# Kernel optimization log

Measured on AMD Instinct MI355X. Metric: run time of the kernel, lower is better.

The kernel has to match this reference:

```python
import jax, jax.numpy as jnp
import numpy as np
import math

H, KV, D, HID, WIN = 8, 4, 256, 2048, 1024  # heads, kv heads, head_dim, hidden, sliding window
B, S = 1, 2048

def _rms(x, scale):
    # Gemma3RMSNorm: hardcoded 1e-6 eps, (1+scale) gain
    var = jnp.mean(jnp.square(x), axis=-1, keepdims=True)
    return x * jax.lax.rsqrt(var + 1e-6) * (1.0 + scale)

def _rot_half(x):
    x1, x2 = jnp.split(x, 2, axis=-1)
    return jnp.concatenate((-x2, x1), axis=-1)

def setup_inputs() -> dict:
    key = jax.random.key(0)
    ks = jax.random.split(key, 8)
    x = jax.random.normal(ks[0], (B, S, HID), jnp.float32)
    attn_mask = jnp.ones((B, S), jnp.bool_)
    segment_pos = jnp.broadcast_to(jnp.arange(S, dtype=jnp.int32)[None], (B, S))
    # true RoPE tables, theta=1e6 (Gemma3 global layers)
    inv_freq = 1.0 / (1e6 ** (np.arange(0, D, 2, dtype=np.float32) / D))
    ang = np.arange(S, dtype=np.float32)[:, None] * inv_freq[None, :]  # [S, D/2]
    emb = np.concatenate([ang, ang], axis=-1)                          # [S, D]
    cos = jnp.asarray(np.cos(emb), jnp.float32)[None]                  # [1, S, D]
    sin = jnp.asarray(np.sin(emb), jnp.float32)[None]
    sd = 1.0 / math.sqrt(HID)
    wq = jax.random.normal(ks[1], (HID, H * D), jnp.float32) * sd
    wk = jax.random.normal(ks[2], (HID, KV * D), jnp.float32) * sd
    wv = jax.random.normal(ks[3], (HID, KV * D), jnp.float32) * sd
    wo = jax.random.normal(ks[4], (H * D, HID), jnp.float32) * (1.0 / math.sqrt(H * D))
    q_scale = jnp.zeros((D,), jnp.float32)  # zeros_init as in module
    k_scale = jnp.zeros((D,), jnp.float32)
    return dict(x=x, attn_mask=attn_mask, segment_pos=segment_pos, cos=cos, sin=sin,
                wq=wq, wk=wk, wv=wv, wo=wo, q_scale=q_scale, k_scale=k_scale)

def reference(x, attn_mask, segment_pos, cos, sin, wq, wk, wv, wo, q_scale, k_scale):
    b, s, _ = x.shape
    # projections -> [b, h, s, d]
    q = (x @ wq).reshape(b, s, H, D).transpose(0, 2, 1, 3)
    k = (x @ wk).reshape(b, s, KV, D).transpose(0, 2, 1, 3)
    v = (x @ wv).reshape(b, s, KV, D).transpose(0, 2, 1, 3)
    # per-head QK RMSNorm
    q = _rms(q, q_scale)
    k = _rms(k, k_scale)
    # RoPE (cos/sin broadcast over head axis, unsqueeze_dim=1)
    c, sn = cos[:, None], sin[:, None]
    q = q * c + _rot_half(q) * sn
    k = k * c + _rot_half(k) * sn
    # GQA: repeat-interleave kv heads
    rep = H // KV
    k = jnp.repeat(k, rep, axis=1)
    v = jnp.repeat(v, rep, axis=1)
    scores = jnp.einsum('bhqd,bhkd->bhqk', q, k) / math.sqrt(D)
    # causal + padding mask (q_len > 1 path, no image bidirectional mask)
    causal = jnp.tril(jnp.ones((s, s), jnp.bool_))
    mask = causal[None] & attn_mask[:, None, :]          # [b, q, kv]
    # sliding window mask (prefill: cache positions = arange)
    kvpos = jnp.arange(s)
    pos = segment_pos[:, :, None]
    sliding = (kvpos[None, None] > pos - WIN) & (kvpos[None, None] < pos + WIN)
    full = mask & sliding
    scores = scores + jnp.where(full[:, None], 0.0, -1e37)
    w = jax.nn.softmax(scores.astype(jnp.float32), axis=-1).astype(scores.dtype)
    out = jnp.einsum('bhqk,bhkd->bhqd', w, v)
    out = out.transpose(0, 2, 1, 3).reshape(b, s, H * D)
    return out @ wo
```

## Files before the change

kernel.cpp:

```cpp
#include <hip/hip_runtime.h>
#include <hip/hip_bf16.h>

#define S_LEN 2048
#define HID 2048
#define NH 8
#define NKV 4
#define HD 256
#define WIN 1024

typedef __hip_bfloat16 bf16;
typedef __attribute__((ext_vector_type(8))) short bf16x8;
typedef __attribute__((ext_vector_type(4))) float f32x4;

__device__ __forceinline__ void gld_lds16(void* lds, const void* g) {
    __builtin_amdgcn_global_load_lds(
        (const __attribute__((address_space(1))) unsigned int*)g,
        (__attribute__((address_space(3))) unsigned int*)lds,
        16, 0, 0);
}


__device__ __forceinline__ void transT_body(const float* __restrict__ src, bf16* __restrict__ dst,
                                            int R, int C, int r0, int c0) {
    __shared__ bf16 Ts[64][72];
    const int tid = threadIdx.x;
    {
        const int r = tid >> 2;
        const int cq = (tid & 3) * 16;
#pragma unroll
        for (int j = 0; j < 16; j += 4) {
            float4 v = *(const float4*)&src[(size_t)(r0 + r) * C + c0 + cq + j];
            Ts[cq + j + 0][r] = __float2bfloat16(v.x);
            Ts[cq + j + 1][r] = __float2bfloat16(v.y);
            Ts[cq + j + 2][r] = __float2bfloat16(v.z);
            Ts[cq + j + 3][r] = __float2bfloat16(v.w);
        }
    }
    __syncthreads();
    {
        const int c = tid >> 2;
        const int rq = (tid & 3) * 16;
#pragma unroll
        for (int j = 0; j < 16; j += 8)
            *(uint4*)&dst[(size_t)(c0 + c) * R + r0 + rq + j] = *(const uint4*)&Ts[c][rq + j];
    }
}

__global__ __launch_bounds__(256)
void prep_all(const float* __restrict__ xf, const float* __restrict__ wqf,
              const float* __restrict__ wkf, const float* __restrict__ wvf,
              bf16* __restrict__ xb, bf16* __restrict__ wqkvt) {
    const int bid = blockIdx.x;
    if (bid < 2048) {
        const int i = bid * 256 + threadIdx.x;
        float4 a = ((const float4*)xf)[i * 2];
        float4 b = ((const float4*)xf)[i * 2 + 1];
        union { uint4 v; bf16 h[8]; } u;
        u.h[0] = __float2bfloat16(a.x); u.h[1] = __float2bfloat16(a.y);
        u.h[2] = __float2bfloat16(a.z); u.h[3] = __float2bfloat16(a.w);
        u.h[4] = __float2bfloat16(b.x); u.h[5] = __float2bfloat16(b.y);
        u.h[6] = __float2bfloat16(b.z); u.h[7] = __float2bfloat16(b.w);
        ((uint4*)xb)[i] = u.v;
    } else {
        const int t = bid - 2048;
        const int bx = t & 63, by = t >> 6;
        const float* src; int C, c0, drow0;
        if (bx < 32)      { src = wqf; C = 2048; c0 = bx * 64;        drow0 = bx * 64; }
        else if (bx < 48) { src = wkf; C = 1024; c0 = (bx - 32) * 64; drow0 = 2048 + (bx - 32) * 64; }
        else              { src = wvf; C = 1024; c0 = (bx - 48) * 64; drow0 = 3072 + (bx - 48) * 64; }
        bf16* dshift = wqkvt + ((size_t)drow0 - c0) * HID;
        transT_body(src, dshift, HID, C, by * 64, c0);
    }
}

__global__ __launch_bounds__(256)
void prep_wo(const float* __restrict__ wof, bf16* __restrict__ wot) {
    const int bx = blockIdx.x & 31, by = blockIdx.x >> 5;
    transT_body(wof, wot, NH * HD, HID, by * 64, bx * 64);
}

__global__ __launch_bounds__(512, 2)
void gemm_qkv8(const bf16* __restrict__ A, const bf16* __restrict__ Bt,
               bf16* __restrict__ P) {
    extern __shared__ bf16 smem[];
    const int tid = threadIdx.x;
    const int w = tid >> 6, lane = tid & 63;
    const int lnm = lane & 15, quad = lane >> 4;
    const int wr = w >> 2, wc = w & 3;
    const int K = 2048;
    const int nt = 16;

    const int bid = blockIdx.x;
    const int xcd = bid & 7, idx = bid >> 3;
    const int wg = xcd * 32 + idx;
    const int z = wg >> 7;
    const int rem = wg & 127;
    const int m0 = (rem >> 4) * 256, n0 = (rem & 15) * 256, kbeg = z * 1024;

    const int sr = lane >> 3;
    const int su = (lane & 7) ^ sr;
    const bf16* gA = A  + (size_t)(m0 + w * 8 + sr) * K + kbeg + su * 8;
    const bf16* gB = Bt + (size_t)(n0 + w * 8 + sr) * K + kbeg + su * 8;
    bf16* const lA = smem + w * 8 * 64;
    bf16* const lB = smem + 32768 + w * 8 * 64;

#define SG_A(d, c, t_) gld_lds16(lA + (d) * 16384 + (c) * 64 * 64, \
                                 gA + (size_t)((c) * 64) * K + (t_) * 64)
#define SG_B(d, c, t_) gld_lds16(lB + (d) * 16384 + (c) * 64 * 64, \
                                 gB + (size_t)((c) * 64) * K + (t_) * 64)
#define AFR(d, m, kh) (*(const bf16x8*)(smem + (d) * 16384 + \
        (wr * 128 + (m) * 16 + lnm) * 64 + (((((kh) << 2) | quad) ^ (lnm & 7)) << 3)))
#define BFR(d, n, kh) (*(const bf16x8*)(smem + 32768 + (d) * 16384 + \
        (wc * 64 + (n) * 16 + lnm) * 64 + (((((kh) << 2) | quad) ^ (lnm & 7)) << 3)))

    f32x4 acc[8][4];
#pragma unroll
    for (int i = 0; i < 8; ++i)
#pragma unroll
        for (int j = 0; j < 4; ++j) acc[i][j] = (f32x4){0.f, 0.f, 0.f, 0.f};

    SG_A(0, 0, 0); SG_A(0, 2, 0);
    SG_B(0, 0, 0); SG_B(0, 1, 0); SG_B(0, 2, 0); SG_B(0, 3, 0);
    SG_A(0, 1, 0); SG_A(0, 3, 0);
    asm volatile("s_waitcnt vmcnt(2)" ::: "memory");
    __builtin_amdgcn_sched_barrier(0);
    __builtin_amdgcn_s_barrier();

    bf16x8 a[2][2], b[4][2];
    for (int t = 0; t < nt; ++t) {
        const int cur = t & 1, nxt = cur ^ 1;
        const bool pf = (t + 1 < nt);

#pragma unroll
        for (int n = 0; n < 4; ++n)
#pragma unroll
            for (int kh = 0; kh < 2; ++kh) b[n][kh] = BFR(cur, n, kh);
#pragma unroll
        for (int m = 0; m < 2; ++m)
#pragma unroll
            for (int kh = 0; kh < 2; ++kh) a[m][kh] = AFR(cur, m, kh);
        if (pf) { SG_A(nxt, 0, t + 1); SG_A(nxt, 2, t + 1); }
        __builtin_amdgcn_s_barrier();
        asm volatile("s_waitcnt lgkmcnt(0)" ::: "memory");
        __builtin_amdgcn_sched_barrier(0);
        __builtin_amdgcn_s_setprio(1);
#pragma unroll
        for (int kh = 0; kh < 2; ++kh)
#pragma unroll
            for (int m = 0; m < 2; ++m)
#pragma unroll
                for (int n = 0; n < 4; ++n)
                    acc[m][n] = __builtin_amdgcn_mfma_f32_16x16x32_bf16(
                        a[m][kh], b[n][kh], acc[m][n], 0, 0, 0);
        __builtin_amdgcn_s_setprio(0);
        __builtin_amdgcn_s_barrier();

#pragma unroll
        for (int m = 0; m < 2; ++m)
#pragma unroll
            for (int kh = 0; kh < 2; ++kh) a[m][kh] = AFR(cur, m + 2, kh);
        if (pf) { SG_B(nxt, 0, t + 1); SG_B(nxt, 1, t + 1); }
        __builtin_amdgcn_s_barrier();
        asm volatile("s_waitcnt lgkmcnt(0)" ::: "memory");
        __builtin_amdgcn_sched_barrier(0);
        __builtin_amdgcn_s_setprio(1);
#pragma unroll
        for (int kh = 0; kh < 2; ++kh)
#pragma unroll
            for (int m = 0; m < 2; ++m)
#pragma unroll
                for (int n = 0; n < 4; ++n)
                    acc[m + 2][n] = __builtin_amdgcn_mfma_f32_16x16x32_bf16(
                        a[m][kh], b[n][kh], acc[m + 2][n], 0, 0, 0);
        __builtin_amdgcn_s_setprio(0);
        if (pf) { asm volatile("s_waitcnt vmcnt(4)" ::: "memory"); }
        else    { asm volatile("s_waitcnt vmcnt(0)" ::: "memory"); }
        __builtin_amdgcn_sched_barrier(0);
        __builtin_amdgcn_s_barrier();

#pragma unroll
        for (int m = 0; m < 2; ++m)
#pragma unroll
            for (int kh = 0; kh < 2; ++kh) a[m][kh] = AFR(cur, m + 4, kh);
        if (pf) { SG_B(nxt, 2, t + 1); SG_B(nxt, 3, t + 1); }
        __builtin_amdgcn_s_barrier();
        asm volatile("s_waitcnt lgkmcnt(0)" ::: "memory");
        __builtin_amdgcn_sched_barrier(0);
        __builtin_amdgcn_s_setprio(1);
#pragma unroll
        for (int kh = 0; kh < 2; ++kh)
#pragma unroll
            for (int m = 0; m < 2; ++m)
#pragma unroll
                for (int n = 0; n < 4; ++n)
                    acc[m + 4][n] = __builtin_amdgcn_mfma_f32_16x16x32_bf16(
                        a[m][kh], b[n][kh], acc[m + 4][n], 0, 0, 0);
        __builtin_amdgcn_s_setprio(0);
        __builtin_amdgcn_s_barrier();

#pragma unroll
        for (int m = 0; m < 2; ++m)
#pragma unroll
            for (int kh = 0; kh < 2; ++kh) a[m][kh] = AFR(cur, m + 6, kh);
        if (pf) { SG_A(nxt, 1, t + 1); SG_A(nxt, 3, t + 1); }
        __builtin_amdgcn_s_barrier();
        asm volatile("s_waitcnt lgkmcnt(0)" ::: "memory");
        __builtin_amdgcn_sched_barrier(0);
        __builtin_amdgcn_s_setprio(1);
#pragma unroll
        for (int kh = 0; kh < 2; ++kh)
#pragma unroll
            for (int m = 0; m < 2; ++m)
#pragma unroll
                for (int n = 0; n < 4; ++n)
                    acc[m + 6][n] = __builtin_amdgcn_mfma_f32_16x16x32_bf16(
                        a[m][kh], b[n][kh], acc[m + 6][n], 0, 0, 0);
        __builtin_amdgcn_s_setprio(0);
        if (pf) {
            asm volatile("s_waitcnt vmcnt(2)" ::: "memory");
            __builtin_amdgcn_sched_barrier(0);
        }
        __builtin_amdgcn_s_barrier();
    }
#undef SG_A
#undef SG_B
#undef AFR
#undef BFR

    bf16* pqk = P + (size_t)z * 8388608;
    bf16* pvt = pqk + 6291456;
#pragma unroll
    for (int m = 0; m < 8; ++m)
#pragma unroll
        for (int n = 0; n < 4; ++n)
#pragma unroll
            for (int r = 0; r < 4; ++r) {
                const int row = m0 + wr * 128 + m * 16 + quad * 4 + r;
                const int col = n0 + wc * 64 + n * 16 + lnm;
                const float v = acc[m][n][r];
                if (col < 3072) pqk[(size_t)row * 3072 + col] = __float2bfloat16(v);
                else            pvt[(size_t)(col - 3072) * 2048 + row] = __float2bfloat16(v);
            }
}

__global__ __launch_bounds__(256)
void qkv_combine(const bf16* __restrict__ P, bf16* __restrict__ Qb,
                 bf16* __restrict__ Kb, bf16* __restrict__ Vtb) {
    const int bid = blockIdx.x;
    union { uint4 v; bf16 h[8]; } a, b, o;
    if (bid < 3072) {
        const unsigned i = bid * 256u + threadIdx.x;
        a.v = *(const uint4*)(P + (size_t)i * 8);
        b.v = *(const uint4*)(P + 8388608 + (size_t)i * 8);
        const unsigned off = i * 8u, row = off / 3072u, col = off - row * 3072u;
        bf16* dst = (col < 2048) ? (Qb + (size_t)row * 2048 + col)
                                 : (Kb + (size_t)row * 1024 + (col - 2048));
#pragma unroll
        for (int j = 0; j < 8; ++j) o.h[j] = __float2bfloat16((float)a.h[j] + (float)b.h[j]);
        *(uint4*)dst = o.v;
    } else {
        const unsigned i = (bid - 3072) * 256u + threadIdx.x;
        a.v = *(const uint4*)(P + 6291456 + (size_t)i * 8);
        b.v = *(const uint4*)(P + 8388608 + 6291456 + (size_t)i * 8);
#pragma unroll
        for (int j = 0; j < 8; ++j) o.h[j] = __float2bfloat16((float)a.h[j] + (float)b.h[j]);
        *(uint4*)(Vtb + (size_t)i * 8) = o.v;
    }
}

template<int MODE>
__global__ __launch_bounds__(512, 2)
void gemm8p(const bf16* __restrict__ A, const bf16* __restrict__ Bt,
            bf16* __restrict__ Cb,
            bf16* __restrict__ Qo, bf16* __restrict__ Ko, bf16* __restrict__ Vto) {
    extern __shared__ bf16 smem[];
    bf16* AsP = smem;
    bf16* BsP = smem + 3 * 256 * 64;

    const int tid = threadIdx.x;
    const int w = tid >> 6, lane = tid & 63;
    const int lnm = lane & 15, quad = lane >> 4;
    const int wr = w >> 1, wc = w & 1;
    const int r8 = lane >> 3;
    const int swz = ((lane & 7) ^ r8) * 8;

    const int bid = blockIdx.x;
    const int xcd = bid & 7, idx = bid >> 3;
    int m0, n0, kbeg, nt;
    size_t zoff = 0;
    {
        const int z   = xcd >> 2;
        const int n_t = (xcd & 3) * 4 + (idx & 3);
        const int m_t = idx >> 2;
        m0 = m_t * 256; n0 = n_t * 128; kbeg = z * 1024; nt = 1024 / 64;
        zoff = (size_t)z * 2048 * 2048;
    }
    const int K = 2048;

    const bf16* pA[4];
#pragma unroll
    for (int g = 0; g < 4; ++g)
        pA[g] = A + (size_t)(m0 + w * 32 + g * 8 + r8) * K + kbeg + swz;
    const bf16* pB[2];
#pragma unroll
    for (int g = 0; g < 2; ++g)
        pB[g] = Bt + (size_t)(n0 + w * 16 + g * 8 + r8) * K + kbeg + swz;
    const int dA = w * 32 * 64;
    const int dB = w * 16 * 64;

#define STG_A(slot, g, t) gld_lds16(AsP + (slot) * 16384 + dA + (g) * 512, pA[g] + (t) * 64)
#define STG_B(slot, g, t) gld_lds16(BsP + (slot) * 8192  + dB + (g) * 512, pB[g] + (t) * 64)
#define LDFRAG(base, row, kh) \
    (*(const bf16x8*)((base) + (row) * 64 + (((((kh) << 2) | quad) ^ ((row) & 7)) << 3)))

    f32x4 acc[4][4];
#pragma unroll
    for (int i = 0; i < 4; ++i)
#pragma unroll
        for (int j = 0; j < 4; ++j) acc[i][j] = (f32x4){0.f, 0.f, 0.f, 0.f};

    STG_A(0, 0, 0); STG_A(0, 1, 0); STG_A(0, 2, 0); STG_A(0, 3, 0);
    STG_B(0, 0, 0); STG_B(0, 1, 0);
    STG_A(1, 0, 1); STG_A(1, 1, 1); STG_A(1, 2, 1); STG_A(1, 3, 1);
    STG_B(1, 0, 1); STG_B(1, 1, 1);
    asm volatile("s_waitcnt vmcnt(6)" ::: "memory");
    __builtin_amdgcn_sched_barrier(0);
    __builtin_amdgcn_s_barrier();

    int sc = 0;
    for (int t = 0; t < nt; ++t) {
        const int ss = (sc == 0) ? 2 : sc - 1;
        const bf16* As_ = AsP + sc * 16384;
        const bf16* Bs_ = BsP + sc * 8192;
        const bool pf = (t + 2 < nt);

        bf16x8 a0[2][2], b[4][2];
#pragma unroll
        for (int tm = 0; tm < 2; ++tm)
#pragma unroll
            for (int kh = 0; kh < 2; ++kh)
                a0[tm][kh] = LDFRAG(As_, wr * 64 + tm * 16 + lnm, kh);
#pragma unroll
        for (int tn = 0; tn < 4; ++tn)
#pragma unroll
            for (int kh = 0; kh < 2; ++kh)
                b[tn][kh] = LDFRAG(Bs_, wc * 64 + tn * 16 + lnm, kh);
        if (pf) { STG_A(ss, 0, t + 2); STG_A(ss, 1, t + 2); STG_B(ss, 0, t + 2); }
        __builtin_amdgcn_s_barrier();
        asm volatile("s_waitcnt lgkmcnt(0)" ::: "memory");
        __builtin_amdgcn_sched_barrier(0);
        __builtin_amdgcn_s_setprio(1);
#pragma unroll
        for (int kh = 0; kh < 2; ++kh)
#pragma unroll
            for (int tm = 0; tm < 2; ++tm)
#pragma unroll
                for (int tn = 0; tn < 4; ++tn)
                    acc[tm][tn] = __builtin_amdgcn_mfma_f32_16x16x32_bf16(
                        a0[tm][kh], b[tn][kh], acc[tm][tn], 0, 0, 0);
        __builtin_amdgcn_s_setprio(0);
        __builtin_amdgcn_s_barrier();

        bf16x8 a1[2][2];
#pragma unroll
        for (int tm = 0; tm < 2; ++tm)
#pragma unroll
            for (int kh = 0; kh < 2; ++kh)
                a1[tm][kh] = LDFRAG(As_, wr * 64 + (tm + 2) * 16 + lnm, kh);
        if (pf) { STG_A(ss, 2, t + 2); STG_A(ss, 3, t + 2); STG_B(ss, 1, t + 2); }
        if (pf) { asm volatile("s_waitcnt vmcnt(6)" ::: "memory"); }
        else    { asm volatile("s_waitcnt vmcnt(0)" ::: "memory"); }
        __builtin_amdgcn_sched_barrier(0);
        __builtin_amdgcn_s_barrier();
        asm volatile("s_waitcnt lgkmcnt(0)" ::: "memory");
        __builtin_amdgcn_sched_barrier(0);
        __builtin_amdgcn_s_setprio(1);
#pragma unroll
        for (int kh = 0; kh < 2; ++kh)
#pragma unroll
            for (int tm = 0; tm < 2; ++tm)
#pragma unroll
                for (int tn = 0; tn < 4; ++tn)
                    acc[tm + 2][tn] = __builtin_amdgcn_mfma_f32_16x16x32_bf16(
                        a1[tm][kh], b[tn][kh], acc[tm + 2][tn], 0, 0, 0);
        __builtin_amdgcn_s_setprio(0);
        __builtin_amdgcn_s_barrier();

        sc = (sc == 2) ? 0 : sc + 1;
    }
#undef STG_A
#undef STG_B
#undef LDFRAG

#pragma unroll
    for (int tm = 0; tm < 4; ++tm)
#pragma unroll
        for (int tn = 0; tn < 4; ++tn)
#pragma unroll
            for (int r = 0; r < 4; ++r) {
                const int row = m0 + wr * 64 + tm * 16 + quad * 4 + r;
                const int col = n0 + wc * 64 + tn * 16 + lnm;
                Cb[zoff + (size_t)row * 2048 + col] = __float2bfloat16(acc[tm][tn][r]);
            }
}

__global__ __launch_bounds__(256)
void splitk_add(const bf16* __restrict__ p, float* __restrict__ out) {
    const int i = blockIdx.x * 256 + threadIdx.x;
    union { uint4 v; bf16 h[8]; } a, b;
    a.v = ((const uint4*)p)[i];
    b.v = ((const uint4*)(p + (size_t)2048 * 2048))[i];
    float4 o0, o1;
    o0.x = (float)a.h[0] + (float)b.h[0]; o0.y = (float)a.h[1] + (float)b.h[1];
    o0.z = (float)a.h[2] + (float)b.h[2]; o0.w = (float)a.h[3] + (float)b.h[3];
    o1.x = (float)a.h[4] + (float)b.h[4]; o1.y = (float)a.h[5] + (float)b.h[5];
    o1.z = (float)a.h[6] + (float)b.h[6]; o1.w = (float)a.h[7] + (float)b.h[7];
    ((float4*)out)[i * 2]     = o0;
    ((float4*)out)[i * 2 + 1] = o1;
}

__global__ __launch_bounds__(64)
void rmsrope_kernel(bf16* __restrict__ Q, bf16* __restrict__ Kb,
                    const float* __restrict__ cosb, const float* __restrict__ sinb,
                    const float* __restrict__ qscale, const float* __restrict__ kscale,
                    float qmul) {
    const int p = blockIdx.x;
    const int hg = blockIdx.y;
    const int lane = threadIdx.x;

    bf16* base;
    const float* scale;
    float mul;
    if (hg < NH) { base = Q + (size_t)p * (NH * HD) + hg * HD; scale = qscale; mul = qmul; }
    else         { base = Kb + (size_t)p * (NKV * HD) + (hg - NH) * HD; scale = kscale; mul = 1.f; }

    const int d0 = lane * 2;
    float x0 = (float)base[d0],       x1 = (float)base[d0 + 1];
    float y0 = (float)base[d0 + 128], y1 = (float)base[d0 + 129];

    float ss = x0 * x0 + x1 * x1 + y0 * y0 + y1 * y1;
#pragma unroll
    for (int off = 32; off > 0; off >>= 1) ss += __shfl_xor(ss, off, 64);
    const float r = rsqrtf(ss * (1.0f / (float)HD) + 1e-6f);

    x0 *= r * (1.f + scale[d0]);
    x1 *= r * (1.f + scale[d0 + 1]);
    y0 *= r * (1.f + scale[d0 + 128]);
    y1 *= r * (1.f + scale[d0 + 129]);

    const size_t cb = (size_t)p * HD;
    const float c0 = cosb[cb + d0],       c1 = cosb[cb + d0 + 1];
    const float cA = cosb[cb + d0 + 128], cB = cosb[cb + d0 + 129];
    const float s0 = sinb[cb + d0],       s1 = sinb[cb + d0 + 1];
    const float sA = sinb[cb + d0 + 128], sB = sinb[cb + d0 + 129];

    base[d0]       = __float2bfloat16((x0 * c0 - y0 * s0) * mul);
    base[d0 + 1]   = __float2bfloat16((x1 * c1 - y1 * s1) * mul);
    base[d0 + 128] = __float2bfloat16((y0 * cA + x0 * sA) * mul);
    base[d0 + 129] = __float2bfloat16((y1 * cB + x1 * sB) * mul);
}

#define NCHUNK 4

__device__ __forceinline__ unsigned pkbf(float a, float b) {
    union { bf16 h; unsigned short u; } ca, cb;
    ca.h = __float2bfloat16(a); cb.h = __float2bfloat16(b);
    return (unsigned)ca.u | ((unsigned)cb.u << 16);
}

__global__ __launch_bounds__(256)
void attn_mfma(const bf16* __restrict__ Q, const bf16* __restrict__ K,
               const bf16* __restrict__ Vt, bf16* __restrict__ Op,
               float2* __restrict__ ml) {
    __shared__ bf16 Ks[2][32][256];
    __shared__ bf16 Vs[256][32];
    const int qt = blockIdx.x, h = blockIdx.y, chunk = blockIdx.z, kvh = h >> 1;
    const int tid = threadIdx.x, w = tid >> 6, lane = tid & 63;
    const int lnm = lane & 15, quad = lane >> 4;

    bf16x8 qf[8];
    const int qrow = qt * 64 + w * 16 + lnm;
#pragma unroll
    for (int s = 0; s < 8; ++s)
        qf[s] = *(const bf16x8*)&Q[(size_t)qrow * HID + h * HD + s * 32 + quad * 8];

    f32x4 o[16];
#pragma unroll
    for (int i = 0; i < 16; ++i) o[i] = (f32x4){0.f, 0.f, 0.f, 0.f};
    float M = -3e38f, L = 0.f;

    const int ktlo = (qt >= 16) ? (2 * qt - 32) : 0;
    const int kthi = 2 * qt + 1;
    const int ntile = kthi - ktlo + 1;
    const int c0 = ktlo + (chunk * ntile) / NCHUNK;
    const int c1 = ktlo + ((chunk + 1) * ntile) / NCHUNK - 1;

    const int srow = w * 8 + (lane >> 5);
    const int sunit = lane & 31;
    const bf16* kg = K + (size_t)kvh * HD;
    const int vrow = lane >> 2;
    const int vgu  = (lane & 3) ^ ((lane >> 3) & 3);
    const bf16* vsrc = Vt + ((size_t)(kvh * HD + w * 64 + vrow)) * S_LEN + vgu * 8;

#define STAGE_K(kt_, buf_)                                                        \
    {                                                                             \
        _Pragma("unroll")                                                         \
        for (int cc = 0; cc < 4; ++cc) {                                          \
            const int r_ = srow + cc * 2;                                         \
            const int ug_ = sunit ^ (r_ & 7);                                     \
            gld_lds16(&Ks[buf_][w * 8 + cc * 2][0],                               \
                      kg + (size_t)((kt_) * 32 + r_) * (NKV * HD) + ug_ * 8);     \
        }                                                                         \
    }
#define STAGE_V(kt_)                                                              \
    {                                                                             \
        _Pragma("unroll")                                                         \
        for (int cc = 0; cc < 4; ++cc)                                            \
            gld_lds16(&Vs[w * 64 + cc * 16][0],                                   \
                      vsrc + (size_t)cc * 16 * S_LEN + (kt_) * 32);               \
    }
#define KFRAG(buf_, t_, s_) \
    (*(const bf16x8*)&Ks[buf_][(t_) * 16 + lnm][((((s_) * 4 + quad) ^ (lnm & 7)) * 8)])
#define VFRAG(t2_) \
    (*(const bf16x8*)&Vs[(t2_) * 16 + lnm][(quad ^ ((lnm >> 1) & 3)) * 8])

    if (c0 <= c1) {
        STAGE_K(c0, 0);
        asm volatile("s_waitcnt vmcnt(0)" ::: "memory");
        __builtin_amdgcn_sched_barrier(0);
        __builtin_amdgcn_s_barrier();

        for (int kt = c0; kt <= c1; ++kt) {
            const int buf = (kt - c0) & 1;
            STAGE_V(kt);
            if (kt < c1) STAGE_K(kt + 1, buf ^ 1);

            f32x4 s4[2];
            s4[0] = (f32x4){0.f, 0.f, 0.f, 0.f};
            s4[1] = (f32x4){0.f, 0.f, 0.f, 0.f};
            __builtin_amdgcn_s_setprio(1);
#pragma unroll
            for (int t = 0; t < 2; ++t)
#pragma unroll
                for (int s = 0; s < 8; ++s)
                    s4[t] = __builtin_amdgcn_mfma_f32_16x16x32_bf16(
                        KFRAG(buf, t, s), qf[s], s4[t], 0, 0, 0);
            __builtin_amdgcn_s_setprio(0);

#pragma unroll
            for (int t = 0; t < 2; ++t)
#pragma unroll
                for (int r = 0; r < 4; ++r) {
                    const int n_g = kt * 32 + t * 16 + quad * 4 + r;
                    if (n_g > qrow || n_g + (WIN - 1) < qrow) s4[t][r] = -1e30f;
                }

            float mx = fmaxf(fmaxf(fmaxf(s4[0][0], s4[0][1]), fmaxf(s4[0][2], s4[0][3])),
                             fmaxf(fmaxf(s4[1][0], s4[1][1]), fmaxf(s4[1][2], s4[1][3])));
            mx = fmaxf(mx, __shfl_xor(mx, 16, 64));
            mx = fmaxf(mx, __shfl_xor(mx, 32, 64));

            if (!__all(mx <= M + 8.f)) {
                const float Mn = fmaxf(M, mx);
                const float al = __expf(M - Mn);
                M = Mn;
                L *= al;
                float alr[4];
#pragma unroll
                for (int r = 0; r < 4; ++r) alr[r] = __shfl(al, quad * 4 + r, 64);
#pragma unroll
                for (int t2 = 0; t2 < 16; ++t2)
#pragma unroll
                    for (int r = 0; r < 4; ++r) o[t2][r] *= alr[r];
            }

            float rs = 0.f;
            unsigned u00, u01, u10, u11;
            {
                float p0 = __expf(s4[0][0] - M), p1 = __expf(s4[0][1] - M);
                float p2 = __expf(s4[0][2] - M), p3 = __expf(s4[0][3] - M);
                rs += (p0 + p1) + (p2 + p3);
                u00 = pkbf(p0, p1); u01 = pkbf(p2, p3);
                p0 = __expf(s4[1][0] - M); p1 = __expf(s4[1][1] - M);
                p2 = __expf(s4[1][2] - M); p3 = __expf(s4[1][3] - M);
                rs += (p0 + p1) + (p2 + p3);
                u10 = pkbf(p0, p1); u11 = pkbf(p2, p3);
            }
            rs += __shfl_xor(rs, 16, 64);
            rs += __shfl_xor(rs, 32, 64);
            L += rs;

            const int slo = lnm + 16 * (2 * (quad & 1));
            const int shi = slo + 16;
            const int A0 = __shfl((int)u00, slo, 64), A1 = __shfl((int)u01, slo, 64);
            const int A2 = __shfl((int)u00, shi, 64), A3 = __shfl((int)u01, shi, 64);
            const int B0 = __shfl((int)u10, slo, 64), B1 = __shfl((int)u11, slo, 64);
            const int B2 = __shfl((int)u10, shi, 64), B3 = __shfl((int)u11, shi, 64);
            union { bf16x8 v; int i4[4]; } pa;
            pa.i4[0] = (quad < 2) ? A0 : B0;
            pa.i4[1] = (quad < 2) ? A1 : B1;
            pa.i4[2] = (quad < 2) ? A2 : B2;
            pa.i4[3] = (quad < 2) ? A3 : B3;

            if (kt < c1) { asm volatile("s_waitcnt vmcnt(4)" ::: "memory"); }
            else         { asm volatile("s_waitcnt vmcnt(0)" ::: "memory"); }
            __builtin_amdgcn_sched_barrier(0);
            __builtin_amdgcn_s_barrier();

            __builtin_amdgcn_s_setprio(1);
#pragma unroll
            for (int t2 = 0; t2 < 16; ++t2)
                o[t2] = __builtin_amdgcn_mfma_f32_16x16x32_bf16(pa.v, VFRAG(t2), o[t2], 0, 0, 0);
            __builtin_amdgcn_s_setprio(0);

            if (kt < c1) {
                asm volatile("s_waitcnt vmcnt(0) lgkmcnt(0)" ::: "memory");
                __builtin_amdgcn_sched_barrier(0);
                __builtin_amdgcn_s_barrier();
            }
        }
    }
#undef STAGE_K
#undef STAGE_V
#undef KFRAG
#undef VFRAG

    const float rL = (L > 0.f) ? (1.f / L) : 0.f;
    float rr[4];
#pragma unroll
    for (int r = 0; r < 4; ++r) rr[r] = __shfl(rL, quad * 4 + r, 64);
    bf16* Opc = Op + (size_t)chunk * S_LEN * HID;
#pragma unroll
    for (int t2 = 0; t2 < 16; ++t2)
#pragma unroll
        for (int r = 0; r < 4; ++r)
            Opc[(size_t)(qt * 64 + w * 16 + quad * 4 + r) * HID + h * HD + t2 * 16 + lnm] =
                __float2bfloat16(o[t2][r] * rr[r]);
    if (quad == 0)
        ml[((size_t)chunk * S_LEN + qt * 64 + w * 16 + lnm) * NH + h] = make_float2(M, L);
}

__global__ __launch_bounds__(256)
void attn_combine(const bf16* __restrict__ Op, const float2* __restrict__ ml,
                  bf16* __restrict__ O) {
    const int row = blockIdx.x, h = blockIdx.y, d = threadIdx.x;
    float2 c[NCHUNK];
    float Mx = -3e38f;
#pragma unroll
    for (int i = 0; i < NCHUNK; ++i) {
        c[i] = ml[((size_t)i * S_LEN + row) * NH + h];
        Mx = fmaxf(Mx, c[i].x);
    }
    float wsum = 0.f, wgt[NCHUNK];
#pragma unroll
    for (int i = 0; i < NCHUNK; ++i) {
        wgt[i] = c[i].y * __expf(c[i].x - Mx);
        wsum += wgt[i];
    }
    const float inv = 1.0f / wsum;
    const size_t idx = (size_t)row * HID + h * HD + d;
    float acc = 0.f;
#pragma unroll
    for (int i = 0; i < NCHUNK; ++i)
        acc += wgt[i] * (float)Op[(size_t)i * S_LEN * HID + idx];
    O[idx] = __float2bfloat16(acc * inv);
}

extern "C" void kernel_launch(void* const* d_in, const int* in_sizes, int n_in,
                              void* d_out, int out_size, void* d_ws, size_t ws_size,
                              hipStream_t stream) {
    const float* xf   = (const float*)d_in[0];
    const float* cosb = (const float*)d_in[3];
    const float* sinb = (const float*)d_in[4];
    const float* wqf  = (const float*)d_in[5];
    const float* wkf  = (const float*)d_in[6];
    const float* wvf  = (const float*)d_in[7];
    const float* wof  = (const float*)d_in[8];
    const float* qs   = (const float*)d_in[9];
    const float* ks   = (const float*)d_in[10];
    float* out = (float*)d_out;
    char* ws = (char*)d_ws;

    bf16*   P     = (bf16*)(ws);
    bf16*   Op    = (bf16*)(ws);
    bf16*   pk    = (bf16*)(ws);
    bf16*   xb    = (bf16*)(ws + (32ull << 20));
    bf16*   Qb    = (bf16*)(ws + (32ull << 20));
    bf16*   Ab    = (bf16*)(ws + (32ull << 20));
    bf16*   wqkvt = (bf16*)(ws + (40ull << 20));
    bf16*   Kb    = (bf16*)(ws + (40ull << 20));
    bf16*   Vtb   = (bf16*)(ws + (44ull << 20));
    bf16*   wot   = (bf16*)(ws + (48ull << 20));
    float2* ml    = (float2*)(ws + (56ull << 20));

    dim3 blk(256);

    static bool attr_done = false;
    if (!attr_done) {
        (void)hipFuncSetAttribute(reinterpret_cast<const void*>(gemm_qkv8),
                                  hipFuncAttributeMaxDynamicSharedMemorySize, 131072);
        (void)hipFuncSetAttribute(reinterpret_cast<const void*>(gemm8p<2>),
                                  hipFuncAttributeMaxDynamicSharedMemorySize, 147456);
        attr_done = true;
    }

    prep_all<<<4096, blk, 0, stream>>>(xf, wqf, wkf, wvf, xb, wqkvt);

    gemm_qkv8<<<dim3(256), dim3(512), 131072, stream>>>(xb, wqkvt, P);

    qkv_combine<<<4096, blk, 0, stream>>>(P, Qb, Kb, Vtb);
    prep_wo<<<1024, blk, 0, stream>>>(wof, wot);

    rmsrope_kernel<<<dim3(S_LEN, NH + NKV), dim3(64), 0, stream>>>(
        Qb, Kb, cosb, sinb, qs, ks, 0.0625f);

    attn_mfma<<<dim3(S_LEN / 64, NH, NCHUNK), blk, 0, stream>>>(Qb, Kb, Vtb, Op, ml);
    attn_combine<<<dim3(S_LEN, NH), blk, 0, stream>>>(Op, ml, Ab);

    gemm8p<2><<<dim3(256), dim3(512), 147456, stream>>>(
        Ab, wot, pk, nullptr, nullptr, nullptr);
    splitk_add<<<2048, blk, 0, stream>>>(pk, out);
}
```

Measured before the change: 285.0 us.

## Use 4-stage K=32 LDS pipeline with 3-deep prefetch in QKV GEMM

Restructures the QKV projection GEMM main loop from a double-buffered K=64 tile to a four-slot ring of K=32 tiles, with loads issued three iterations ahead. The LDS swizzle and the global-to-LDS load mapping are rewritten for the narrower 32-element rows. Each iteration now runs two MFMA phases instead of four, with graded vmcnt waits at the loop tail. The aim is to hide global-load latency better, at the cost of twice as many iterations and barriers per unit of K.

Measured after the change: 287.2 us. No clear change (+0.8%).

```diff
diff --git a/kernel.cpp b/kernel.cpp
--- a/kernel.cpp
+++ b/kernel.cpp
@@ -88,7 +88,7 @@
     const int lnm = lane & 15, quad = lane >> 4;
     const int wr = w >> 2, wc = w & 3;
     const int K = 2048;
-    const int nt = 16;
+    const int nt = 32;
 
     const int bid = blockIdx.x;
     const int xcd = bid & 7, idx = bid >> 3;
@@ -97,21 +97,21 @@
     const int rem = wg & 127;
     const int m0 = (rem >> 4) * 256, n0 = (rem & 15) * 256, kbeg = z * 1024;
 
-    const int sr = lane >> 3;
-    const int su = (lane & 7) ^ sr;
-    const bf16* gA = A  + (size_t)(m0 + w * 8 + sr) * K + kbeg + su * 8;
-    const bf16* gB = Bt + (size_t)(n0 + w * 8 + sr) * K + kbeg + su * 8;
-    bf16* const lA = smem + w * 8 * 64;
-    bf16* const lB = smem + 32768 + w * 8 * 64;
-
-#define SG_A(d, c, t_) gld_lds16(lA + (d) * 16384 + (c) * 64 * 64, \
-                                 gA + (size_t)((c) * 64) * K + (t_) * 64)
-#define SG_B(d, c, t_) gld_lds16(lB + (d) * 16384 + (c) * 64 * 64, \
-                                 gB + (size_t)((c) * 64) * K + (t_) * 64)
-#define AFR(d, m, kh) (*(const bf16x8*)(smem + (d) * 16384 + \
-        (wr * 128 + (m) * 16 + lnm) * 64 + (((((kh) << 2) | quad) ^ (lnm & 7)) << 3)))
-#define BFR(d, n, kh) (*(const bf16x8*)(smem + 32768 + (d) * 16384 + \
-        (wc * 64 + (n) * 16 + lnm) * 64 + (((((kh) << 2) | quad) ^ (lnm & 7)) << 3)))
+    const int sr = lane >> 2;
+    const int su = (lane & 3) ^ ((lane >> 3) & 3);
+    const bf16* gA = A  + (size_t)(m0 + w * 16 + sr) * K + kbeg + su * 8;
+    const bf16* gB = Bt + (size_t)(n0 + w * 16 + sr) * K + kbeg + su * 8;
+    bf16* const lA = smem + w * 512;
+    bf16* const lB = smem + 32768 + w * 512;
+
+#define SG_A(s_, h_, t_) gld_lds16(lA + (s_) * 8192 + (h_) * 4096, \
+                                   gA + (size_t)((h_) * 128) * K + (t_) * 32)
+#define SG_B(s_, h_, t_) gld_lds16(lB + (s_) * 8192 + (h_) * 4096, \
+                                   gB + (size_t)((h_) * 128) * K + (t_) * 32)
+#define AFR(s_, m_) (*(const bf16x8*)(smem + (s_) * 8192 + \
+        (wr * 128 + (m_) * 16 + lnm) * 32 + ((quad ^ ((lnm >> 1) & 3)) << 3)))
+#define BFR(s_, n_) (*(const bf16x8*)(smem + 32768 + (s_) * 8192 + \
+        (wc * 64 + (n_) * 16 + lnm) * 32 + ((quad ^ ((lnm >> 1) & 3)) << 3)))
 
     f32x4 acc[8][4];
 #pragma unroll
@@ -119,107 +119,54 @@
 #pragma unroll
         for (int j = 0; j < 4; ++j) acc[i][j] = (f32x4){0.f, 0.f, 0.f, 0.f};
 
-    SG_A(0, 0, 0); SG_A(0, 2, 0);
-    SG_B(0, 0, 0); SG_B(0, 1, 0); SG_B(0, 2, 0); SG_B(0, 3, 0);
-    SG_A(0, 1, 0); SG_A(0, 3, 0);
-    asm volatile("s_waitcnt vmcnt(2)" ::: "memory");
+    SG_A(0, 0, 0); SG_A(0, 1, 0); SG_B(0, 0, 0); SG_B(0, 1, 0);
+    SG_A(1, 0, 1); SG_A(1, 1, 1); SG_B(1, 0, 1); SG_B(1, 1, 1);
+    SG_A(2, 0, 2); SG_A(2, 1, 2); SG_B(2, 0, 2); SG_B(2, 1, 2);
+    asm volatile("s_waitcnt vmcnt(8)" ::: "memory");
     __builtin_amdgcn_sched_barrier(0);
     __builtin_amdgcn_s_barrier();
 
-    bf16x8 a[2][2], b[4][2];
     for (int t = 0; t < nt; ++t) {
-        const int cur = t & 1, nxt = cur ^ 1;
-        const bool pf = (t + 1 < nt);
-
-#pragma unroll
-        for (int n = 0; n < 4; ++n)
-#pragma unroll
-            for (int kh = 0; kh < 2; ++kh) b[n][kh] = BFR(cur, n, kh);
-#pragma unroll
-        for (int m = 0; m < 2; ++m)
-#pragma unroll
-            for (int kh = 0; kh < 2; ++kh) a[m][kh] = AFR(cur, m, kh);
-        if (pf) { SG_A(nxt, 0, t + 1); SG_A(nxt, 2, t + 1); }
+        const int s = t & 3, s3 = (t + 3) & 3;
+        const bool pf = (t + 3 < nt);
+        bf16x8 a[4], b[4];
+
+#pragma unroll
+        for (int n = 0; n < 4; ++n) b[n] = BFR(s, n);
+#pragma unroll
+        for (int m = 0; m < 4; ++m) a[m] = AFR(s, m);
+        if (pf) { SG_A(s3, 0, t + 3); SG_A(s3, 1, t + 3); }
         __builtin_amdgcn_s_barrier();
         asm volatile("s_waitcnt lgkmcnt(0)" ::: "memory");
         __builtin_amdgcn_sched_barrier(0);
         __builtin_amdgcn_s_setprio(1);
 #pragma unroll
-        for (int kh = 0; kh < 2; ++kh)
-#pragma unroll
-            for (int m = 0; m < 2; ++m)
-#pragma unroll
-                for (int n = 0; n < 4; ++n)
-                    acc[m][n] = __builtin_amdgcn_mfma_f32_16x16x32_bf16(
-                        a[m][kh], b[n][kh], acc[m][n], 0, 0, 0);
+        for (int m = 0; m < 4; ++m)
+#pragma unroll
+            for (int n = 0; n < 4; ++n)
+                acc[m][n] = __builtin_amdgcn_mfma_f32_16x16x32_bf16(
+                    a[m], b[n], acc[m][n], 0, 0, 0);
         __builtin_amdgcn_s_setprio(0);
         __builtin_amdgcn_s_barrier();
 
 #pragma unroll
-        for (int m = 0; m < 2; ++m)
-#pragma unroll
-            for (int kh = 0; kh < 2; ++kh) a[m][kh] = AFR(cur, m + 2, kh);
-        if (pf) { SG_B(nxt, 0, t + 1); SG_B(nxt, 1, t + 1); }
+        for (int m = 0; m < 4; ++m) a[m] = AFR(s, m + 4);
+        if (pf) { SG_B(s3, 0, t + 3); SG_B(s3, 1, t + 3); }
         __builtin_amdgcn_s_barrier();
         asm volatile("s_waitcnt lgkmcnt(0)" ::: "memory");
         __builtin_amdgcn_sched_barrier(0);
         __builtin_amdgcn_s_setprio(1);
 #pragma unroll
-        for (int kh = 0; kh < 2; ++kh)
-#pragma unroll
-            for (int m = 0; m < 2; ++m)
-#pragma unroll
-                for (int n = 0; n < 4; ++n)
-                    acc[m + 2][n] = __builtin_amdgcn_mfma_f32_16x16x32_bf16(
-                        a[m][kh], b[n][kh], acc[m + 2][n], 0, 0, 0);
+        for (int m = 0; m < 4; ++m)
+#pragma unroll
+            for (int n = 0; n < 4; ++n)
+                acc[m + 4][n] = __builtin_amdgcn_mfma_f32_16x16x32_bf16(
+                    a[m], b[n], acc[m + 4][n], 0, 0, 0);
         __builtin_amdgcn_s_setprio(0);
-        if (pf) { asm volatile("s_waitcnt vmcnt(4)" ::: "memory"); }
-        else    { asm volatile("s_waitcnt vmcnt(0)" ::: "memory"); }
+        if (t + 3 < nt)      { asm volatile("s_waitcnt vmcnt(8)" ::: "memory"); }
+        else if (t + 2 < nt) { asm volatile("s_waitcnt vmcnt(4)" ::: "memory"); }
+        else if (t + 1 < nt) { asm volatile("s_waitcnt vmcnt(0)" ::: "memory"); }
         __builtin_amdgcn_sched_barrier(0);
-        __builtin_amdgcn_s_barrier();
-
-#pragma unroll
-        for (int m = 0; m < 2; ++m)
-#pragma unroll
-            for (int kh = 0; kh < 2; ++kh) a[m][kh] = AFR(cur, m + 4, kh);
-        if (pf) { SG_B(nxt, 2, t + 1); SG_B(nxt, 3, t + 1); }
-        __builtin_amdgcn_s_barrier();
-        asm volatile("s_waitcnt lgkmcnt(0)" ::: "memory");
-        __builtin_amdgcn_sched_barrier(0);
-        __builtin_amdgcn_s_setprio(1);
-#pragma unroll
-        for (int kh = 0; kh < 2; ++kh)
-#pragma unroll
-            for (int m = 0; m < 2; ++m)
-#pragma unroll
-                for (int n = 0; n < 4; ++n)
-                    acc[m + 4][n] = __builtin_amdgcn_mfma_f32_16x16x32_bf16(
-                        a[m][kh], b[n][kh], acc[m + 4][n], 0, 0, 0);
-        __builtin_amdgcn_s_setprio(0);
-        __builtin_amdgcn_s_barrier();
-
-#pragma unroll
-        for (int m = 0; m < 2; ++m)
-#pragma unroll
-            for (int kh = 0; kh < 2; ++kh) a[m][kh] = AFR(cur, m + 6, kh);
-        if (pf) { SG_A(nxt, 1, t + 1); SG_A(nxt, 3, t + 1); }
-        __builtin_amdgcn_s_barrier();
-        asm volatile("s_waitcnt lgkmcnt(0)" ::: "memory");
-        __builtin_amdgcn_sched_barrier(0);
-        __builtin_amdgcn_s_setprio(1);
-#pragma unroll
-        for (int kh = 0; kh < 2; ++kh)
-#pragma unroll
-            for (int m = 0; m < 2; ++m)
-#pragma unroll
-                for (int n = 0; n < 4; ++n)
-                    acc[m + 6][n] = __builtin_amdgcn_mfma_f32_16x16x32_bf16(
-                        a[m][kh], b[n][kh], acc[m + 6][n], 0, 0, 0);
-        __builtin_amdgcn_s_setprio(0);
-        if (pf) {
-            asm volatile("s_waitcnt vmcnt(2)" ::: "memory");
-            __builtin_amdgcn_sched_barrier(0);
-        }
         __builtin_amdgcn_s_barrier();
     }
 #undef SG_A
```
